# Kernel optimization log

Hardware: AMD Instinct MI355X
Metric: run time of the kernel (lower is better)

The kernel has to match this reference:

```python
import jax, jax.numpy as jnp
import numpy as np

NEG = -1.0e9

def setup_inputs() -> dict:
    key = jax.random.key(0)
    ks = jax.random.split(key, 4)
    B, S, D, DK = 4, 2048, 1024, 128
    inputs = jax.random.normal(ks[0], (B, S, D), dtype=jnp.float32)
    scale = 1.0 / np.sqrt(D)
    Wq = jax.random.normal(ks[1], (D, DK), dtype=jnp.float32) * scale
    Wk = jax.random.normal(ks[2], (D, DK), dtype=jnp.float32) * scale
    Wv = jax.random.normal(ks[3], (D, DK), dtype=jnp.float32) * scale
    bq = jnp.zeros((DK,), dtype=jnp.float32)
    bk = jnp.zeros((DK,), dtype=jnp.float32)
    bv = jnp.zeros((DK,), dtype=jnp.float32)
    return {"inputs": inputs, "Wq": Wq, "bq": bq, "Wk": Wk, "bk": bk, "Wv": Wv, "bv": bv}

def reference(inputs, Wq, bq, Wk, bk, Wv, bv):
    # Q/K/V projections: Dense(d_k) on last dim
    Q = jnp.einsum('bsd,dk->bsk', inputs, Wq) + bq
    K = jnp.einsum('bsd,dk->bsk', inputs, Wk) + bk
    V = jnp.einsum('bsd,dk->bsk', inputs, Wv) + bv
    d_k = Q.shape[-1]
    S = inputs.shape[1]
    # FAITHFUL to original bug: mask = lower-triangular ones, added *-1e9
    # (masks the lower triangle including the diagonal, NOT the upper).
    mask = jnp.tril(jnp.ones((S, S), dtype=inputs.dtype))
    scores = jnp.einsum('bqk,bsk->bqs', Q, K) / jnp.sqrt(jnp.asarray(d_k, inputs.dtype))
    masked_scores = scores + mask * NEG  # [B, S, S]
    attn = jax.nn.softmax(masked_scores, axis=-1)
    out = jnp.einsum('bqs,bsk->bqk', attn, V)  # [B, S, d_k]
    return out
```

## Files before the change

kernel.cpp:

```cpp
#include <hip/hip_runtime.h>
#include <hip/hip_bf16.h>

typedef __attribute__((ext_vector_type(8))) short bf16x8;
typedef __attribute__((ext_vector_type(4))) float f32x4;

#define QSCALE 0.088388347648318447f

__device__ __forceinline__ unsigned short f2bf(float f) {
  __hip_bfloat16 h = __float2bfloat16(f);
  unsigned short u;
  __builtin_memcpy(&u, &h, 2);
  return u;
}
__device__ __forceinline__ float bf2f(unsigned short u) {
  unsigned int x = ((unsigned int)u) << 16;
  float f; __builtin_memcpy(&f, &x, 4);
  return f;
}

__device__ __forceinline__ void gload_lds16(void* lds, const void* g) {
  __builtin_amdgcn_global_load_lds(
      (const __attribute__((address_space(1))) unsigned int*)g,
      (__attribute__((address_space(3))) unsigned int*)lds, 16, 0, 0);
}

__global__ __launch_bounds__(256) void cvt(const float* __restrict__ x,
                                           unsigned short* __restrict__ xb,
                                           const float* __restrict__ Wq,
                                           const float* __restrict__ Wk,
                                           const float* __restrict__ Wv,
                                           unsigned short* __restrict__ Wt) {
  const int bid = blockIdx.x;
  if (bid < 4096) {
    int i = (bid * 256 + threadIdx.x) * 8;
    float4 v0 = *reinterpret_cast<const float4*>(x + i);
    float4 v1 = *reinterpret_cast<const float4*>(x + i + 4);
    ushort4 o0, o1;
    o0.x = f2bf(v0.x); o0.y = f2bf(v0.y); o0.z = f2bf(v0.z); o0.w = f2bf(v0.w);
    o1.x = f2bf(v1.x); o1.y = f2bf(v1.y); o1.z = f2bf(v1.z); o1.w = f2bf(v1.w);
    *reinterpret_cast<ushort4*>(xb + i) = o0;
    *reinterpret_cast<ushort4*>(xb + i + 4) = o1;
  } else {
    int idx = (bid - 4096) * 256 + threadIdx.x;
    int n = idx >> 10, d = idx & 1023;
    const float* W = (n < 128) ? Wq : (n < 256 ? Wk : Wv);
    float v = W[d * 128 + (n & 127)];
    if (n < 128) v *= QSCALE;
    Wt[idx] = f2bf(v);
  }
}

__global__ __launch_bounds__(256) void proj_gemm(
    const unsigned short* __restrict__ Xb, const unsigned short* __restrict__ Wt,
    const float* __restrict__ bq, const float* __restrict__ bk, const float* __restrict__ bv,
    unsigned short* __restrict__ Qb, unsigned short* __restrict__ Kb,
    unsigned short* __restrict__ Vt) {
  __shared__ unsigned short sA[64 * 64];
  __shared__ unsigned short sB[64 * 64];
  const int nt = blockIdx.x % 6;
  const int mt = blockIdx.x / 6;
  const int m0 = mt * 64;
  const int n0 = nt * 64;
  const int tid = threadIdx.x;
  const int lane = tid & 63;
  const int w = tid >> 6;
  const int r = lane & 15, g = lane >> 4;
  const int wm = (w >> 1) * 32, wn = (w & 1) * 32;

  f32x4 acc[2][2];
  #pragma unroll
  for (int mi = 0; mi < 2; ++mi)
    #pragma unroll
    for (int ni = 0; ni < 2; ++ni)
      acc[mi][ni] = (f32x4){0.f, 0.f, 0.f, 0.f};

  const char* Ab = (const char*)Xb;
  const char* Bb = (const char*)Wt;
  char* sAb = (char*)sA;
  char* sBb = (char*)sB;

  for (int k0 = 0; k0 < 1024; k0 += 64) {
    #pragma unroll
    for (int j = 0; j < 2; ++j) {
      int f = j * 4096 + tid * 16;
      int row = f >> 7;
      int colb = f & 127;
      gload_lds16(sAb + f, Ab + ((size_t)(m0 + row) * 1024 + k0) * 2 + colb);
      gload_lds16(sBb + f, Bb + ((size_t)(n0 + row) * 1024 + k0) * 2 + colb);
    }
    __syncthreads();
    #pragma unroll
    for (int kk = 0; kk < 2; ++kk) {
      bf16x8 af[2], bfr[2];
      #pragma unroll
      for (int mi = 0; mi < 2; ++mi)
        af[mi] = *reinterpret_cast<const bf16x8*>(sA + (wm + mi * 16 + r) * 64 + kk * 32 + g * 8);
      #pragma unroll
      for (int ni = 0; ni < 2; ++ni)
        bfr[ni] = *reinterpret_cast<const bf16x8*>(sB + (wn + ni * 16 + r) * 64 + kk * 32 + g * 8);
      #pragma unroll
      for (int mi = 0; mi < 2; ++mi)
        #pragma unroll
        for (int ni = 0; ni < 2; ++ni)
          acc[mi][ni] = __builtin_amdgcn_mfma_f32_16x16x32_bf16(af[mi], bfr[ni], acc[mi][ni], 0, 0, 0);
    }
    __syncthreads();
  }

  const float* bias = (nt < 2) ? bq : (nt < 4 ? bk : bv);
  const float bsc = (nt < 2) ? QSCALE : 1.0f;
  #pragma unroll
  for (int mi = 0; mi < 2; ++mi) {
    #pragma unroll
    for (int ni = 0; ni < 2; ++ni) {
      const int colg = n0 + wn + ni * 16 + r;
      const int colm = colg & 127;
      const float bias_v = bias[colm] * bsc;
      #pragma unroll
      for (int e = 0; e < 4; ++e) {
        const int row = m0 + wm + mi * 16 + g * 4 + e;
        const unsigned short hh = f2bf(acc[mi][ni][e] + bias_v);
        if (nt < 2) Qb[(size_t)row * 128 + colm] = hh;
        else if (nt < 4) Kb[(size_t)row * 128 + colm] = hh;
        else {
          const int bb = row >> 11, s = row & 2047;
          Vt[((size_t)bb * 128 + colm) * 2048 + s] = hh;
        }
      }
    }
  }
}

__global__ __launch_bounds__(512, 4) void attn(
    const unsigned short* __restrict__ Qb, const unsigned short* __restrict__ Kb,
    const unsigned short* __restrict__ Vt,
    unsigned short* __restrict__ po, float* __restrict__ pl) {
  __shared__ char sK[2][8192];
  __shared__ char sV[2][8192];
  __shared__ unsigned short pbuf_s[8][512];
  const int tid = threadIdx.x;
  const int lane = tid & 63;
  const int w = tid >> 6;
  const int r = lane & 15, g = lane >> 4;
  const int sig = blockIdx.x & 7;
  const int b = (blockIdx.x >> 3) & 3;
  const int p = blockIdx.x >> 5;

  const char* Kg = (const char*)(Kb + (size_t)b * 2048 * 128);
  const char* Vg = (const char*)(Vt + (size_t)b * 128 * 2048);
  unsigned short* pbuf = pbuf_s[w];

  const int krow = tid >> 4;
  const int kcol = ((tid & 15) * 16) ^ ((krow & 7) * 16);
  const int vrow = tid >> 2;
  const int vcol = ((tid & 3) * 16) ^ ((vrow & 3) * 16);

  for (int phase = 0; phase < 2; ++phase) {
    const int t = phase ? (15 - p) : p;
    const int q0b = t << 7;
    const int ntiles = (2048 - q0b) >> 5;
    const int q0w = q0b + w * 16;

    const unsigned short* Q = Qb + (size_t)(b * 2048 + q0w) * 128;
    bf16x8 qf[4];
    #pragma unroll
    for (int kk = 0; kk < 4; ++kk)
      qf[kk] = *reinterpret_cast<const bf16x8*>(Q + r * 128 + kk * 32 + g * 8);

    f32x4 o[8];
    #pragma unroll
    for (int ni = 0; ni < 8; ++ni) o[ni] = (f32x4){0.f, 0.f, 0.f, 0.f};
    float l[4];
    #pragma unroll
    for (int e = 0; e < 4; ++e) l[e] = 0.f;

    const int nT = (ntiles > sig) ? ((ntiles - sig + 7) >> 3) : 0;

    if (nT > 0) {
      const int s0 = q0b + (sig << 5);
      gload_lds16(&sK[0][tid * 16], Kg + (size_t)(s0 + krow) * 256 + kcol);
      gload_lds16(&sV[0][tid * 16], Vg + (size_t)vrow * 4096 + (size_t)s0 * 2 + vcol);
    }
    for (int it = 0; it < nT; ++it) {
      const int cur = it & 1;
      const int s0 = q0b + ((sig + (it << 3)) << 5);
      if (it + 1 < nT) {
        const int s1 = s0 + 256;
        gload_lds16(&sK[cur ^ 1][tid * 16], Kg + (size_t)(s1 + krow) * 256 + kcol);
        gload_lds16(&sV[cur ^ 1][tid * 16], Vg + (size_t)vrow * 4096 + (size_t)s1 * 2 + vcol);
        asm volatile("s_waitcnt vmcnt(2)" ::: "memory");
      } else {
        asm volatile("s_waitcnt vmcnt(0)" ::: "memory");
      }
      asm volatile("s_barrier" ::: "memory");

      f32x4 st[2];
      #pragma unroll
      for (int sj = 0; sj < 2; ++sj) {
        f32x4 a = (f32x4){0.f, 0.f, 0.f, 0.f};
        #pragma unroll
        for (int kk = 0; kk < 4; ++kk) {
          const bf16x8 kf = *reinterpret_cast<const bf16x8*>(
              &sK[cur][(sj * 16 + r) * 256 + (((kk * 64 + g * 16) ^ ((r & 7) * 16)))]);
          a = __builtin_amdgcn_mfma_f32_16x16x32_bf16(qf[kk], kf, a, 0, 0, 0);
        }
        st[sj] = a;
      }
      #pragma unroll
      for (int sj = 0; sj < 2; ++sj) {
        const int s = s0 + sj * 16 + r;
        #pragma unroll
        for (int e = 0; e < 4; ++e) {
          const int q = q0w + g * 4 + e;
          st[sj][e] = (s <= q) ? 0.f : __expf(st[sj][e]);
        }
      }
      #pragma unroll
      for (int e = 0; e < 4; ++e) l[e] += st[0][e] + st[1][e];

      #pragma unroll
      for (int sj = 0; sj < 2; ++sj)
        #pragma unroll
        for (int e = 0; e < 4; ++e)
          pbuf[(g * 4 + e) * 32 + sj * 16 + r] = f2bf(st[sj][e]);
      asm volatile("s_waitcnt lgkmcnt(0)" ::: "memory");
      __builtin_amdgcn_sched_barrier(0);
      const bf16x8 pa = *reinterpret_cast<const bf16x8*>(&pbuf[r * 32 + g * 8]);

      #pragma unroll
      for (int ni = 0; ni < 8; ++ni) {
        const bf16x8 vf = *reinterpret_cast<const bf16x8*>(
            &sV[cur][(ni * 16 + r) * 64 + ((g * 16) ^ ((r & 3) * 16))]);
        o[ni] = __builtin_amdgcn_mfma_f32_16x16x32_bf16(pa, vf, o[ni], 0, 0, 0);
      }
      asm volatile("s_waitcnt lgkmcnt(0)" ::: "memory");
      __builtin_amdgcn_sched_barrier(0);
      asm volatile("s_barrier" ::: "memory");
    }

    #pragma unroll
    for (int off = 1; off < 16; off <<= 1)
      #pragma unroll
      for (int e = 0; e < 4; ++e)
        l[e] += __shfl_xor(l[e], off, 64);

    const size_t pb = ((size_t)((b * 16 + t) * 8 + sig)) * 16384;
    #pragma unroll
    for (int ni = 0; ni < 8; ++ni)
      #pragma unroll
      for (int e = 0; e < 4; ++e)
        po[pb + (size_t)(w * 16 + g * 4 + e) * 128 + ni * 16 + r] = f2bf(o[ni][e]);
    if (r == 0) {
      #pragma unroll
      for (int e = 0; e < 4; ++e)
        pl[((size_t)((b * 16 + t) * 8 + sig)) * 128 + w * 16 + g * 4 + e] = l[e];
    }
  }
}

__global__ __launch_bounds__(256) void combine(const unsigned short* __restrict__ po,
                                               const float* __restrict__ pl,
                                               const unsigned short* __restrict__ Vt,
                                               float* __restrict__ out) {
  const int bid = blockIdx.x;
  if (bid < 4096) {
    const int idx = bid * 256 + threadIdx.x;
    const int d = idx & 127;
    const int gq = idx >> 7;
    const int b = gq >> 11, q = gq & 2047;
    if (q == 2047) return;
    const int qt = q >> 7, row = q & 127;
    const size_t base = (size_t)(b * 16 + qt) * 8;
    float o = 0.f, l = 0.f;
    #pragma unroll
    for (int s = 0; s < 8; ++s) {
      o += bf2f(po[(base + s) * 16384 + row * 128 + d]);
      l += pl[(base + s) * 128 + row];
    }
    out[idx] = (l > 0.f) ? o / l : 0.f;
  } else {
    const int seg = bid - 4096;
    const int b = seg >> 5;
    const int w = threadIdx.x >> 6;
    const int lane = threadIdx.x & 63;
    const int dk = (seg & 31) * 4 + w;
    const unsigned short* row = Vt + (size_t)(b * 128 + dk) * 2048;
    float s = 0.f;
    for (int i = lane; i < 2048; i += 64) s += bf2f(row[i]);
    #pragma unroll
    for (int off = 32; off > 0; off >>= 1) s += __shfl_down(s, off, 64);
    if (lane == 0) out[(size_t)(b * 2048 + 2047) * 128 + dk] = s * (1.0f / 2048.0f);
  }
}

extern "C" void kernel_launch(void* const* d_in, const int* in_sizes, int n_in,
                              void* d_out, int out_size, void* d_ws, size_t ws_size,
                              hipStream_t stream) {
  const float* x  = (const float*)d_in[0];
  const float* Wq = (const float*)d_in[1];
  const float* bq = (const float*)d_in[2];
  const float* Wk = (const float*)d_in[3];
  const float* bk = (const float*)d_in[4];
  const float* Wv = (const float*)d_in[5];
  const float* bv = (const float*)d_in[6];
  float* out = (float*)d_out;
  char* ws = (char*)d_ws;
  unsigned short* Xb = (unsigned short*)(ws);
  unsigned short* Wt = (unsigned short*)(ws + (size_t)(16u << 20));
  unsigned short* Qb = (unsigned short*)(ws + (size_t)(17u << 20));
  unsigned short* Kb = (unsigned short*)(ws + (size_t)(19u << 20));
  unsigned short* Vt = (unsigned short*)(ws + (size_t)(21u << 20));
  unsigned short* po = (unsigned short*)(ws + (size_t)(24u << 20));
  float* pl = (float*)(ws + (size_t)(48u << 20));

  hipLaunchKernelGGL(cvt, dim3(5632), dim3(256), 0, stream, x, Xb, Wq, Wk, Wv, Wt);
  hipLaunchKernelGGL(proj_gemm, dim3(768), dim3(256), 0, stream,
                     Xb, Wt, bq, bk, bv, Qb, Kb, Vt);
  hipLaunchKernelGGL(attn, dim3(256), dim3(512), 0, stream, Qb, Kb, Vt, po, pl);
  hipLaunchKernelGGL(combine, dim3(4224), dim3(256), 0, stream, po, pl, Vt, out);
}
```

Measured before the change: 64.64 us.

## Split attention query tile across two 256-thread blocks with per-block KV start

The attention kernel now runs 512 blocks of 4 waves instead of 256 blocks of 8 waves. Each block handles 64 query rows of a 128-row tile, and each thread issues two K and two V async loads per stage. The second half-tile starts its key range at its own offset, so the masked upper-triangle work is trimmed a little. The loop now has a single barrier per iteration, placed before the next prefetch, instead of two. In exchange, K/V tiles are loaded twice, once by each half-block, which raises global traffic, and per-block LDS use stays about the same.

```diff
diff --git a/kernel.cpp b/kernel.cpp
--- a/kernel.cpp
+++ b/kernel.cpp
@@ -131,35 +131,40 @@
   }
 }
 
-__global__ __launch_bounds__(512, 4) void attn(
+__global__ __launch_bounds__(256, 4) void attn(
     const unsigned short* __restrict__ Qb, const unsigned short* __restrict__ Kb,
     const unsigned short* __restrict__ Vt,
     unsigned short* __restrict__ po, float* __restrict__ pl) {
   __shared__ char sK[2][8192];
   __shared__ char sV[2][8192];
-  __shared__ unsigned short pbuf_s[8][512];
+  __shared__ unsigned short pbuf_s[4][512];
   const int tid = threadIdx.x;
   const int lane = tid & 63;
   const int w = tid >> 6;
   const int r = lane & 15, g = lane >> 4;
   const int sig = blockIdx.x & 7;
   const int b = (blockIdx.x >> 3) & 3;
-  const int p = blockIdx.x >> 5;
+  const int p = (blockIdx.x >> 5) & 7;
+  const int h2 = blockIdx.x >> 8;
 
   const char* Kg = (const char*)(Kb + (size_t)b * 2048 * 128);
   const char* Vg = (const char*)(Vt + (size_t)b * 128 * 2048);
   unsigned short* pbuf = pbuf_s[w];
 
-  const int krow = tid >> 4;
-  const int kcol = ((tid & 15) * 16) ^ ((krow & 7) * 16);
-  const int vrow = tid >> 2;
-  const int vcol = ((tid & 3) * 16) ^ ((vrow & 3) * 16);
+  const int kr0 = tid >> 4;
+  const int kr1 = 16 + (tid >> 4);
+  const int kc0 = ((tid & 15) * 16) ^ ((kr0 & 7) * 16);
+  const int kc1 = ((tid & 15) * 16) ^ ((kr1 & 7) * 16);
+  const int vr0 = tid >> 2;
+  const int vr1 = 64 + (tid >> 2);
+  const int vc0 = ((tid & 3) * 16) ^ ((vr0 & 3) * 16);
+  const int vc1 = ((tid & 3) * 16) ^ ((vr1 & 3) * 16);
 
   for (int phase = 0; phase < 2; ++phase) {
     const int t = phase ? (15 - p) : p;
-    const int q0b = t << 7;
-    const int ntiles = (2048 - q0b) >> 5;
-    const int q0w = q0b + w * 16;
+    const int sb = t * 128 + h2 * 64;
+    const int ntiles = (2048 - sb) >> 5;
+    const int q0w = t * 128 + h2 * 64 + w * 16;
 
     const unsigned short* Q = Qb + (size_t)(b * 2048 + q0w) * 128;
     bf16x8 qf[4];
@@ -177,22 +182,25 @@
     const int nT = (ntiles > sig) ? ((ntiles - sig + 7) >> 3) : 0;
 
     if (nT > 0) {
-      const int s0 = q0b + (sig << 5);
-      gload_lds16(&sK[0][tid * 16], Kg + (size_t)(s0 + krow) * 256 + kcol);
-      gload_lds16(&sV[0][tid * 16], Vg + (size_t)vrow * 4096 + (size_t)s0 * 2 + vcol);
+      const int s0 = sb + (sig << 5);
+      gload_lds16(&sK[0][tid * 16], Kg + (size_t)(s0 + kr0) * 256 + kc0);
+      gload_lds16(&sK[0][4096 + tid * 16], Kg + (size_t)(s0 + kr1) * 256 + kc1);
+      gload_lds16(&sV[0][tid * 16], Vg + (size_t)vr0 * 4096 + (size_t)s0 * 2 + vc0);
+      gload_lds16(&sV[0][4096 + tid * 16], Vg + (size_t)vr1 * 4096 + (size_t)s0 * 2 + vc1);
     }
     for (int it = 0; it < nT; ++it) {
       const int cur = it & 1;
-      const int s0 = q0b + ((sig + (it << 3)) << 5);
+      const int s0 = sb + ((sig + (it << 3)) << 5);
+      asm volatile("s_waitcnt vmcnt(0) lgkmcnt(0)" ::: "memory");
+      __builtin_amdgcn_sched_barrier(0);
+      asm volatile("s_barrier" ::: "memory");
       if (it + 1 < nT) {
         const int s1 = s0 + 256;
-        gload_lds16(&sK[cur ^ 1][tid * 16], Kg + (size_t)(s1 + krow) * 256 + kcol);
-        gload_lds16(&sV[cur ^ 1][tid * 16], Vg + (size_t)vrow * 4096 + (size_t)s1 * 2 + vcol);
-        asm volatile("s_waitcnt vmcnt(2)" ::: "memory");
-      } else {
-        asm volatile("s_waitcnt vmcnt(0)" ::: "memory");
-      }
-      asm volatile("s_barrier" ::: "memory");
+        gload_lds16(&sK[cur ^ 1][tid * 16], Kg + (size_t)(s1 + kr0) * 256 + kc0);
+        gload_lds16(&sK[cur ^ 1][4096 + tid * 16], Kg + (size_t)(s1 + kr1) * 256 + kc1);
+        gload_lds16(&sV[cur ^ 1][tid * 16], Vg + (size_t)vr0 * 4096 + (size_t)s1 * 2 + vc0);
+        gload_lds16(&sV[cur ^ 1][4096 + tid * 16], Vg + (size_t)vr1 * 4096 + (size_t)s1 * 2 + vc1);
+      }
 
       f32x4 st[2];
       #pragma unroll
@@ -233,9 +241,6 @@
             &sV[cur][(ni * 16 + r) * 64 + ((g * 16) ^ ((r & 3) * 16))]);
         o[ni] = __builtin_amdgcn_mfma_f32_16x16x32_bf16(pa, vf, o[ni], 0, 0, 0);
       }
-      asm volatile("s_waitcnt lgkmcnt(0)" ::: "memory");
-      __builtin_amdgcn_sched_barrier(0);
-      asm volatile("s_barrier" ::: "memory");
     }
 
     #pragma unroll
@@ -245,16 +250,18 @@
         l[e] += __shfl_xor(l[e], off, 64);
 
     const size_t pb = ((size_t)((b * 16 + t) * 8 + sig)) * 16384;
+    const int rbase = h2 * 64 + w * 16;
     #pragma unroll
     for (int ni = 0; ni < 8; ++ni)
       #pragma unroll
       for (int e = 0; e < 4; ++e)
-        po[pb + (size_t)(w * 16 + g * 4 + e) * 128 + ni * 16 + r] = f2bf(o[ni][e]);
+        po[pb + (size_t)(rbase + g * 4 + e) * 128 + ni * 16 + r] = f2bf(o[ni][e]);
     if (r == 0) {
       #pragma unroll
       for (int e = 0; e < 4; ++e)
-        pl[((size_t)((b * 16 + t) * 8 + sig)) * 128 + w * 16 + g * 4 + e] = l[e];
-    }
+        pl[((size_t)((b * 16 + t) * 8 + sig)) * 128 + rbase + g * 4 + e] = l[e];
+    }
+    __syncthreads();
   }
 }
 
@@ -316,6 +323,6 @@
   hipLaunchKernelGGL(cvt, dim3(5632), dim3(256), 0, stream, x, Xb, Wq, Wk, Wv, Wt);
   hipLaunchKernelGGL(proj_gemm, dim3(768), dim3(256), 0, stream,
                      Xb, Wt, bq, bk, bv, Qb, Kb, Vt);
-  hipLaunchKernelGGL(attn, dim3(256), dim3(512), 0, stream, Qb, Kb, Vt, po, pl);
+  hipLaunchKernelGGL(attn, dim3(512), dim3(256), 0, stream, Qb, Kb, Vt, po, pl);
   hipLaunchKernelGGL(combine, dim3(4224), dim3(256), 0, stream, po, pl, Vt, out);
 }
```

Measured after the change: 64.08 us. Within noise of the previous version (-0.9%).
